# Optimization experiments

Hardware: AMD Instinct MI355X
Metric: run time of the kernel (lower is better)

Reference implementation:

```python
import jax, jax.numpy as jnp
import numpy as np

B, L, D, H, DH = 2, 2048, 1024, 16, 64
THETA_T = 100.0
EPS_COS = 1e-6
EPS_NORM = 1e-6


def make_rope_tables(n_heads=H, d_head=DH, theta_t=THETA_T):
    dr = d_head // 12                      # 5 rotary freqs per head per axis
    n = n_heads * dr
    log_min, log_max = np.log(np.pi), np.log(10.0 * np.pi)
    f = np.exp(np.linspace(log_min, log_max, n + 1)[:-1])
    freqs = np.stack([f, f]).reshape(2, dr, n_heads).transpose(0, 2, 1)   # (2, H, dr)
    t_freqs = (theta_t ** (-np.arange(n, dtype=np.float64) / n)).reshape(dr, n_heads).T  # (H, dr)
    return jnp.asarray(freqs, jnp.float32), jnp.asarray(t_freqs, jnp.float32)


def rms_norm(x, scale, eps=EPS_NORM):
    ms = jnp.mean(x.astype(jnp.float32) ** 2, axis=-1, keepdims=True)
    return x * (scale.astype(jnp.float32) * jax.lax.rsqrt(ms + eps)).astype(x.dtype)


def rope_theta(pos, pos_orig, time, freqs, t_freqs):
    # pos_to_use: (b, l, c=2, xy=2), mapped to [-1, 1]
    pos_use = jnp.stack([pos_orig, pos], axis=2) * 2.0 - 1.0
    theta_w = pos_use[..., 0][:, :, :, None, None] * freqs[0]      # b l 2 H dr
    theta_h = pos_use[..., 1][:, :, :, None, None] * freqs[1]      # b l 2 H dr
    theta_t = time[:, :, None, None, None] * t_freqs               # b l 1 H dr
    theta = jnp.concatenate([theta_h, theta_w, theta_t], axis=2)   # b l 5 H dr
    b, l = theta.shape[0], theta.shape[1]
    theta = jnp.transpose(theta, (0, 1, 3, 2, 4)).reshape(b, l, H, -1)  # b l H (5*dr)
    return theta


def apply_rotary_emb(x, theta):
    d = theta.shape[-1]
    x1, x2, x3 = x[..., :d], x[..., d:2 * d], x[..., 2 * d:]
    cos, sin = jnp.cos(theta), jnp.sin(theta)
    y1 = x1 * cos - x2 * sin
    y2 = x2 * cos + x1 * sin
    return jnp.concatenate([y1, y2, x3], axis=-1)


def scale_for_cosine_sim(q, k, scale, eps=EPS_COS):
    sq = jnp.sum(q * q, axis=-1, keepdims=True)
    sk = jnp.sum(k * k, axis=-1, keepdims=True)
    sqrt_scale = jnp.sqrt(scale)                         # (H,1,1) -> broadcasts to (b,H,l,1)
    return q * (sqrt_scale * jax.lax.rsqrt(sq + eps)), k * (sqrt_scale * jax.lax.rsqrt(sk + eps))


def setup_inputs() -> dict:
    key = jax.random.key(0)
    ks = jax.random.split(key, 8)
    return {
        "x": jax.random.normal(ks[0], (B, L, D), jnp.float32),
        "pos": jax.random.uniform(ks[1], (B, L, 2), jnp.float32),
        "pos_orig": jax.random.uniform(ks[2], (B, L, 2), jnp.float32),
        "time": jax.random.uniform(ks[3], (B, L), jnp.float32),
        "w_qkv": jax.random.normal(ks[4], (3 * D, D), jnp.float32) * (D ** -0.5),
        "w_out": jax.random.normal(ks[5], (D, D), jnp.float32) * (D ** -0.5),
        "w_up": jax.random.normal(ks[6], (4 * D, D), jnp.float32) * (D ** -0.5),
        "w_down": jax.random.normal(ks[7], (D, 4 * D), jnp.float32) * ((4 * D) ** -0.5),
        "norm1_scale": jnp.ones((D,), jnp.float32),
        "norm2_scale": jnp.ones((D,), jnp.float32),
        "qk_scale": jnp.full((H, 1, 1), 10.0, jnp.float32),
    }


def reference(x, pos, pos_orig, time, w_qkv, w_out, w_up, w_down,
              norm1_scale, norm2_scale, qk_scale):
    freqs, t_freqs = make_rope_tables()
    b, l, _ = x.shape

    # --- attention block (pre-norm) ---
    xn = rms_norm(x, norm1_scale)
    qkv = jnp.einsum('bld,ed->ble', xn, w_qkv)                  # b l 3D
    q, k, v = jnp.split(qkv, 3, axis=-1)
    q = q.reshape(b, l, H, DH)
    k = k.reshape(b, l, H, DH)
    v = v.reshape(b, l, H, DH).transpose(0, 2, 1, 3)            # b H l dh

    theta = rope_theta(pos, pos_orig, time, freqs, t_freqs)      # b l H 25
    q = apply_rotary_emb(q, theta).transpose(0, 2, 1, 3)         # b H l dh
    k = apply_rotary_emb(k, theta).transpose(0, 2, 1, 3)

    q, k = scale_for_cosine_sim(q, k, qk_scale)                  # cosine-sim QK norm
    scores = jnp.einsum('bhqd,bhkd->bhqk', q, k)                 # scale=1 (already folded in)
    probs = jax.nn.softmax(scores, axis=-1)
    attn = jnp.einsum('bhqk,bhkd->bhqd', probs, v)
    attn = attn.transpose(0, 2, 1, 3).reshape(b, l, D)
    x = x + jnp.einsum('bld,ed->ble', attn, w_out)

    h = rms_norm(x, norm2_scale)
    h = jax.nn.gelu(jnp.einsum('bld,ed->ble', h, w_up), approximate=True)
    x = x + jnp.einsum('ble,de->bld', h, w_down)
    return x
```

## Files before the change

### kernel.cpp

```cpp
#include <hip/hip_runtime.h>

#define B_ 2
#define L_ 2048
#define D_ 1024
#define H_ 16
#define DH_ 64

typedef float f32x4 __attribute__((ext_vector_type(4)));
typedef __bf16 bf16x8 __attribute__((ext_vector_type(8)));

__device__ __forceinline__ ushort f2bf(float f) {
  unsigned u = __float_as_uint(f);
  u += 0x7fffu + ((u >> 16) & 1u);
  return (ushort)(u >> 16);
}
__device__ __forceinline__ float bf2f(ushort h) {
  return __uint_as_float(((unsigned)h) << 16);
}

__device__ __forceinline__ void gload_lds16(const void* g, void* l) {
  __builtin_amdgcn_global_load_lds(
      (const __attribute__((address_space(1))) unsigned*)g,
      (__attribute__((address_space(3))) unsigned*)l, 16, 0, 0);
}

__global__ __launch_bounds__(256) void cast_bf16_kernel(const float* __restrict__ in,
                                                        ushort* __restrict__ out, int n4) {
  int i = blockIdx.x * 256 + threadIdx.x;
  if (i >= n4) return;
  float4 v = ((const float4*)in)[i];
  ushort4 o;
  o.x = f2bf(v.x); o.y = f2bf(v.y); o.z = f2bf(v.z); o.w = f2bf(v.w);
  ((ushort4*)out)[i] = o;
}

__global__ __launch_bounds__(256) void rmsnorm_kernel(const float* __restrict__ x,
                                                      const float* __restrict__ scale,
                                                      ushort* __restrict__ out) {
  int row = blockIdx.x, t = threadIdx.x;
  float4 v = ((const float4*)(x + (size_t)row * D_))[t];
  float ss = v.x * v.x + v.y * v.y + v.z * v.z + v.w * v.w;
#pragma unroll
  for (int d = 1; d < 64; d <<= 1) ss += __shfl_xor(ss, d);
  __shared__ float wsum[4];
  if ((t & 63) == 0) wsum[t >> 6] = ss;
  __syncthreads();
  float tot = wsum[0] + wsum[1] + wsum[2] + wsum[3];
  float r = rsqrtf(tot * (1.0f / D_) + 1e-6f);
  float4 sc = ((const float4*)scale)[t];
  ushort4 o;
  o.x = f2bf(v.x * sc.x * r); o.y = f2bf(v.y * sc.y * r);
  o.z = f2bf(v.z * sc.z * r); o.w = f2bf(v.w * sc.w * r);
  ((ushort4*)(out + (size_t)row * D_))[t] = o;
}

template <int EPI, int BM, int BN, int DEPTH, int XR>
__global__ __launch_bounds__(256) void gemm_nt(const ushort* __restrict__ A,
                                               const ushort* __restrict__ Bw,
                                               void* __restrict__ Cout,
                                               const float* __restrict__ resid,
                                               int M, int N, int K) {
  constexpr int WROWS = BM / 2, WCOLS = BN / 2;
  constexpr int MR = WROWS / 16, NR = WCOLS / 16;
  constexpr int ALOADS = BM / 64, BLOADS = BN / 64;
  constexpr int NLOADS = ALOADS + BLOADS;
  constexpr int XC = 8 / XR;
  __shared__ __align__(16) ushort Als[DEPTH][BM * 32];
  __shared__ __align__(16) ushort Bls[DEPTH][BN * 32];
  const int tid = threadIdx.x;
  const int lane = tid & 63;
  const int w = tid >> 6;
  const int wr = w >> 1, wc = w & 1;
  const int bid = blockIdx.y * gridDim.x + blockIdx.x;
  const int xcd = bid & 7;
  const int i = bid >> 3;
  const int CR = gridDim.x / XR, CC = gridDim.y / XC;
  const int rt = (xcd % XR) * CR + (i % CR);
  const int ct = (xcd / XR) * CC + (i / CR);
  const int row0 = rt * BM;
  const int col0 = ct * BN;
  const ushort* Ab = A + (size_t)row0 * K;
  const ushort* Bb = Bw + (size_t)col0 * K;
  const int sr = tid >> 2;
  const int scA = (((tid & 3) ^ ((tid >> 3) & 3)) * 8);
  const int fr = lane & 15;
  const int fg = lane >> 4;
  f32x4 zero = {0.f, 0.f, 0.f, 0.f};
  f32x4 acc[MR][NR];
#pragma unroll
  for (int m = 0; m < MR; m++)
#pragma unroll
    for (int n = 0; n < NR; n++) acc[m][n] = zero;

  auto stage = [&](int buf, int kt) {
#pragma unroll
    for (int i2 = 0; i2 < ALOADS; i2++)
      gload_lds16(Ab + (size_t)(sr + 64 * i2) * K + kt + scA, &Als[buf][i2 * 2048 + tid * 8]);
#pragma unroll
    for (int i2 = 0; i2 < BLOADS; i2++)
      gload_lds16(Bb + (size_t)(sr + 64 * i2) * K + kt + scA, &Bls[buf][i2 * 2048 + tid * 8]);
  };
  const int nt = K >> 5;
#pragma unroll
  for (int p = 0; p < DEPTH - 1; p++) stage(p, p << 5);
  int cur = 0, sbuf = DEPTH - 1;
  for (int t = 0; t < nt; t++) {
    const int ahead = nt - 1 - t;
    if constexpr (DEPTH == 3) {
      if (ahead >= 1) asm volatile("s_waitcnt vmcnt(%0)" ::"i"(NLOADS) : "memory");
      else            asm volatile("s_waitcnt vmcnt(0)" ::: "memory");
    } else {
      if (ahead >= 3)      asm volatile("s_waitcnt vmcnt(%0)" ::"i"(3 * NLOADS) : "memory");
      else if (ahead == 2) asm volatile("s_waitcnt vmcnt(%0)" ::"i"(2 * NLOADS) : "memory");
      else if (ahead == 1) asm volatile("s_waitcnt vmcnt(%0)" ::"i"(NLOADS) : "memory");
      else                 asm volatile("s_waitcnt vmcnt(0)" ::: "memory");
    }
    __builtin_amdgcn_s_barrier();
    __builtin_amdgcn_sched_barrier(0);
    if (t + DEPTH - 1 < nt) {
      stage(sbuf, (t + DEPTH - 1) << 5);
      sbuf = (sbuf == DEPTH - 1) ? 0 : sbuf + 1;
    }
    bf16x8 af[MR], bfr[NR];
#pragma unroll
    for (int m = 0; m < MR; m++) {
      int rA = wr * WROWS + m * 16 + fr;
      af[m] = *(const bf16x8*)&Als[cur][rA * 32 + ((fg ^ ((rA >> 1) & 3)) << 3)];
    }
#pragma unroll
    for (int n = 0; n < NR; n++) {
      int rB = wc * WCOLS + n * 16 + fr;
      bfr[n] = *(const bf16x8*)&Bls[cur][rB * 32 + ((fg ^ ((rB >> 1) & 3)) << 3)];
    }
    __builtin_amdgcn_s_setprio(1);
#pragma unroll
    for (int m = 0; m < MR; m++)
#pragma unroll
      for (int n = 0; n < NR; n++)
        acc[m][n] = __builtin_amdgcn_mfma_f32_16x16x32_bf16(af[m], bfr[n], acc[m][n], 0, 0, 0);
    __builtin_amdgcn_s_setprio(0);
    cur = (cur == DEPTH - 1) ? 0 : cur + 1;
  }
  const int orow = row0 + wr * WROWS + fg * 4;
  const int ocol = col0 + wc * WCOLS + fr;
#pragma unroll
  for (int m = 0; m < MR; m++) {
#pragma unroll
    for (int j = 0; j < 4; j++) {
      int r = orow + m * 16 + j;
#pragma unroll
      for (int n = 0; n < NR; n++) {
        int cidx = ocol + n * 16;
        size_t idx = (size_t)r * N + cidx;
        float v = acc[m][n][j];
        if (EPI == 0) {
          ((ushort*)Cout)[idx] = f2bf(v);
        } else if (EPI == 1) {
          ((float*)Cout)[idx] = resid[idx] + v;
        } else {
          float g = 0.5f * v * (1.0f + tanhf(0.7978845608f * (v + 0.044715f * v * v * v)));
          ((ushort*)Cout)[idx] = f2bf(g);
        }
      }
    }
  }
}

__global__ __launch_bounds__(256) void rope_kernel(const ushort* __restrict__ qkv,
                                                   const float* __restrict__ pos,
                                                   const float* __restrict__ pos_orig,
                                                   const float* __restrict__ timep,
                                                   const float* __restrict__ qk_scale,
                                                   ushort* __restrict__ qr,
                                                   ushort* __restrict__ kr) {
  int gw = (blockIdx.x * 256 + threadIdx.x) >> 6;
  int lane = threadIdx.x & 63;
  int h = gw & 15;
  int row = gw >> 4;
  int b = row >> 11;
  int l = row & (L_ - 1);
  float qv = bf2f(qkv[(size_t)row * 3072 + h * 64 + lane]);
  float kv = bf2f(qkv[(size_t)row * 3072 + 1024 + h * 64 + lane]);
  float c = 1.0f, s = 0.0f;
  if (lane < 50) {
    int idx = lane < 25 ? lane : lane - 25;
    int sg = idx / 5, d = idx % 5;
    int fi = d * 16 + h;
    float th;
    if (sg == 4) {
      th = timep[row] * __expf(-(float)fi * 0.05756462732485115f);
    } else {
      float fr = 3.14159265358979323846f * __expf((float)fi * 0.028782313662425575f);
      const float* psrc = (sg == 0 || sg == 2) ? pos_orig : pos;
      int comp = (sg < 2) ? 1 : 0;
      th = (2.0f * psrc[(size_t)row * 2 + comp] - 1.0f) * fr;
    }
    s = sinf(th);
    c = cosf(th);
  }
  int partner = lane < 25 ? lane + 25 : lane - 25;
  float qp = __shfl(qv, partner, 64);
  float kp = __shfl(kv, partner, 64);
  float yq, yk;
  if (lane < 25) { yq = qv * c - qp * s; yk = kv * c - kp * s; }
  else if (lane < 50) { yq = qv * c + qp * s; yk = kv * c + kp * s; }
  else { yq = qv; yk = kv; }
  float sq = yq * yq, sk = yk * yk;
#pragma unroll
  for (int d = 1; d < 64; d <<= 1) { sq += __shfl_xor(sq, d); sk += __shfl_xor(sk, d); }
  float scl = sqrtf(qk_scale[h]);
  float qo = yq * scl * rsqrtf(sq + 1e-6f);
  float ko = yk * scl * rsqrtf(sk + 1e-6f);
  size_t o = ((size_t)(b * 16 + h) * L_ + l) * 64 + lane;
  qr[o] = f2bf(qo);
  kr[o] = f2bf(ko);
}

__global__ __launch_bounds__(256) void vtrans_kernel(const ushort* __restrict__ qkv,
                                                     ushort* __restrict__ vT) {
  __shared__ __align__(16) ushort tile[64][72];
  int t = threadIdx.x;
  int lt = blockIdx.x;
  int bh = blockIdx.y;
  int b = bh >> 4, h = bh & 15;
  int r = t >> 3, c0 = (t & 7) * 8;
#pragma unroll
  for (int half = 0; half < 2; half++) {
    const ushort* src =
        qkv + (size_t)(b * L_ + lt * 64 + r + half * 32) * 3072 + 2048 + h * 64 + c0;
    *(uint4*)&tile[r + half * 32][c0] = *(const uint4*)src;
  }
  __syncthreads();
#pragma unroll
  for (int half = 0; half < 2; half++) {
    int dh = r + half * 32;
    unsigned p0 = (unsigned)tile[c0 + 0][dh] | ((unsigned)tile[c0 + 1][dh] << 16);
    unsigned p1 = (unsigned)tile[c0 + 2][dh] | ((unsigned)tile[c0 + 3][dh] << 16);
    unsigned p2 = (unsigned)tile[c0 + 4][dh] | ((unsigned)tile[c0 + 5][dh] << 16);
    unsigned p3 = (unsigned)tile[c0 + 6][dh] | ((unsigned)tile[c0 + 7][dh] << 16);
    uint4 o; o.x = p0; o.y = p1; o.z = p2; o.w = p3;
    *(uint4*)&vT[((size_t)bh * 64 + dh) * L_ + lt * 64 + c0] = o;
  }
}

__global__ __launch_bounds__(256) void attn_kernel(const ushort* __restrict__ qr,
                                                   const ushort* __restrict__ kr,
                                                   const ushort* __restrict__ vT,
                                                   ushort* __restrict__ attnb) {
  __shared__ __align__(16) ushort Kls[2][64 * 64];
  __shared__ __align__(16) ushort Vls[2][64 * 64];
  __shared__ __align__(16) ushort Pls[4][16 * 64];
  const int tid = threadIdx.x, lane = tid & 63, w = tid >> 6;
  const int qt = blockIdx.x, bh = blockIdx.y;
  const int b = bh >> 4;
  const int fr = lane & 15, fg = lane >> 4;
  const ushort* Qb = qr + ((size_t)bh * L_ + qt * 64 + w * 16) * 64;
  bf16x8 qf[2];
#pragma unroll
  for (int c = 0; c < 2; c++)
    qf[c] = *(const bf16x8*)(Qb + fr * 64 + c * 32 + fg * 8);
  f32x4 zero = {0.f, 0.f, 0.f, 0.f};
  f32x4 accO[4];
#pragma unroll
  for (int n = 0; n < 4; n++) accO[n] = zero;
  float lrow[4] = {0.f, 0.f, 0.f, 0.f};
  const int sr = tid >> 3;
  const int scz = (((tid & 7) ^ (sr & 7)) * 8);
  auto stage = [&](int buf, int kt) {
    gload_lds16(kr + ((size_t)bh * L_ + kt + sr) * 64 + scz, &Kls[buf][tid * 8]);
    gload_lds16(kr + ((size_t)bh * L_ + kt + 32 + sr) * 64 + scz, &Kls[buf][2048 + tid * 8]);
    gload_lds16(vT + ((size_t)bh * 64 + sr) * L_ + kt + scz, &Vls[buf][tid * 8]);
    gload_lds16(vT + ((size_t)bh * 64 + 32 + sr) * L_ + kt + scz, &Vls[buf][2048 + tid * 8]);
  };
  stage(0, 0);
  int cur = 0;
  for (int t = 0; t < (L_ >> 6); t++) {
    asm volatile("s_waitcnt vmcnt(0)" ::: "memory");
    __builtin_amdgcn_s_barrier();
    __builtin_amdgcn_sched_barrier(0);
    if (t + 1 < (L_ >> 6)) stage(cur ^ 1, (t + 1) << 6);
    f32x4 sv[4];
#pragma unroll
    for (int n = 0; n < 4; n++) sv[n] = zero;
    __builtin_amdgcn_s_setprio(1);
#pragma unroll
    for (int c = 0; c < 2; c++) {
#pragma unroll
      for (int n = 0; n < 4; n++) {
        bf16x8 kf =
            *(const bf16x8*)&Kls[cur][(n * 16 + fr) * 64 + (((c * 4 + fg) ^ (fr & 7)) << 3)];
        sv[n] = __builtin_amdgcn_mfma_f32_16x16x32_bf16(qf[c], kf, sv[n], 0, 0, 0);
      }
    }
    __builtin_amdgcn_s_setprio(0);
#pragma unroll
    for (int n = 0; n < 4; n++)
#pragma unroll
      for (int j = 0; j < 4; j++) {
        float p = __expf(sv[n][j] - 12.0f);
        sv[n][j] = p;
        lrow[j] += p;
      }
#pragma unroll
    for (int j = 0; j < 4; j++) {
      int row = fg * 4 + j;
      int rbase = row * 64;
      int rx = row & 7;
#pragma unroll
      for (int n = 0; n < 4; n++) {
        int chunk = 2 * n + (fr >> 3);
        Pls[w][rbase + ((chunk ^ rx) << 3) + (fr & 7)] =
            (ushort)(__float_as_uint(sv[n][j]) >> 16);
      }
    }
    __builtin_amdgcn_s_setprio(1);
#pragma unroll
    for (int c = 0; c < 2; c++) {
      bf16x8 pa = *(const bf16x8*)&Pls[w][fr * 64 + (((c * 4 + fg) ^ (fr & 7)) << 3)];
#pragma unroll
      for (int n = 0; n < 4; n++) {
        bf16x8 vb =
            *(const bf16x8*)&Vls[cur][(n * 16 + fr) * 64 + (((c * 4 + fg) ^ (fr & 7)) << 3)];
        accO[n] = __builtin_amdgcn_mfma_f32_16x16x32_bf16(pa, vb, accO[n], 0, 0, 0);
      }
    }
    __builtin_amdgcn_s_setprio(0);
    cur ^= 1;
  }
#pragma unroll
  for (int j = 0; j < 4; j++) {
#pragma unroll
    for (int d = 1; d < 16; d <<= 1) lrow[j] += __shfl_xor(lrow[j], d);
    lrow[j] = 1.0f / lrow[j];
  }
#pragma unroll
  for (int n = 0; n < 4; n++) {
#pragma unroll
    for (int j = 0; j < 4; j++) {
      float o = accO[n][j] * lrow[j];
      int qrow = qt * 64 + w * 16 + fg * 4 + j;
      int dh = fr + n * 16;
      attnb[(size_t)(b * L_ + qrow) * 1024 + (bh & 15) * 64 + dh] = f2bf(o);
    }
  }
}

extern "C" void kernel_launch(void* const* d_in, const int* in_sizes, int n_in,
                              void* d_out, int out_size, void* d_ws, size_t ws_size,
                              hipStream_t stream) {
  const float* x = (const float*)d_in[0];
  const float* pos = (const float*)d_in[1];
  const float* pos_orig = (const float*)d_in[2];
  const float* timep = (const float*)d_in[3];
  const float* w_qkv = (const float*)d_in[4];
  const float* w_out = (const float*)d_in[5];
  const float* w_up = (const float*)d_in[6];
  const float* w_down = (const float*)d_in[7];
  const float* norm1 = (const float*)d_in[8];
  const float* norm2 = (const float*)d_in[9];
  const float* qk_scale = (const float*)d_in[10];
  float* out = (float*)d_out;
  char* ws = (char*)d_ws;
  size_t off = 0;
  auto alloc = [&](size_t bytes) {
    void* p = ws + off;
    off += bytes;
    return p;
  };
  ushort* xn = (ushort*)alloc(8ull << 20);
  ushort* qkvb = (ushort*)alloc(32ull << 20);
  ushort* qrb = (ushort*)alloc(8ull << 20);
  ushort* krb = (ushort*)alloc(8ull << 20);
  ushort* vTb = (ushort*)alloc(8ull << 20);
  ushort* attnb = (ushort*)alloc(8ull << 20);
  float* x1 = (float*)alloc(16ull << 20);
  ushort* wqkvb = (ushort*)alloc(6ull << 20);
  ushort* woutb = (ushort*)alloc(2ull << 20);
  ushort* wupb = (ushort*)alloc(8ull << 20);
  ushort* wdownb = (ushort*)alloc(8ull << 20);

  cast_bf16_kernel<<<3072, 256, 0, stream>>>(w_qkv, wqkvb, 3145728 / 4);
  cast_bf16_kernel<<<1024, 256, 0, stream>>>(w_out, woutb, 1048576 / 4);
  cast_bf16_kernel<<<4096, 256, 0, stream>>>(w_up, wupb, 4194304 / 4);
  cast_bf16_kernel<<<4096, 256, 0, stream>>>(w_down, wdownb, 4194304 / 4);

  rmsnorm_kernel<<<4096, 256, 0, stream>>>(x, norm1, xn);
  gemm_nt<0, 128, 128, 3, 4><<<dim3(32, 24), 256, 0, stream>>>(xn, wqkvb, qkvb, nullptr, 4096, 3072, 1024);
  rope_kernel<<<16384, 256, 0, stream>>>(qkvb, pos, pos_orig, timep, qk_scale, qrb, krb);
  vtrans_kernel<<<dim3(32, 32), 256, 0, stream>>>(qkvb, vTb);
  attn_kernel<<<dim3(32, 32), 256, 0, stream>>>(qrb, krb, vTb, attnb);
  gemm_nt<1, 64, 64, 5, 8><<<dim3(64, 16), 256, 0, stream>>>(attnb, woutb, x1, x, 4096, 1024, 1024);
  rmsnorm_kernel<<<4096, 256, 0, stream>>>(x1, norm2, xn);
  gemm_nt<2, 128, 128, 3, 4><<<dim3(32, 32), 256, 0, stream>>>(xn, wupb, qkvb, nullptr, 4096, 4096, 1024);
  gemm_nt<1, 64, 64, 5, 8><<<dim3(64, 16), 256, 0, stream>>>(qkvb, wdownb, out, x1, 4096, 1024, 4096);
}
```

Baseline: 299.4 us.

## Merge weight casts, store residual in bf16, and remap GEMM/attention block order

Replaces the four weight-cast launches with one combined kernel. Stores the intermediate residual x1 as bf16 instead of fp32, so the out-projection epilogue, the second rmsnorm and the down-projection epilogue move less data. Changes the XCD tile-mapping parameters of the out and down GEMMs, with an option to make the column index vary fastest, and remaps attention blocks so consecutive blocks on an XCD share a head. Rounding the residual stream to bf16 loses precision in the final output.

```diff
diff --git a/kernel.cpp b/kernel.cpp
--- a/kernel.cpp
+++ b/kernel.cpp
@@ -24,21 +24,40 @@
       (__attribute__((address_space(3))) unsigned*)l, 16, 0, 0);
 }
 
-__global__ __launch_bounds__(256) void cast_bf16_kernel(const float* __restrict__ in,
-                                                        ushort* __restrict__ out, int n4) {
+__global__ __launch_bounds__(256) void cast_all_kernel(const float* __restrict__ w0,
+                                                       const float* __restrict__ w1,
+                                                       const float* __restrict__ w2,
+                                                       const float* __restrict__ w3,
+                                                       ushort* __restrict__ o0,
+                                                       ushort* __restrict__ o1,
+                                                       ushort* __restrict__ o2,
+                                                       ushort* __restrict__ o3) {
   int i = blockIdx.x * 256 + threadIdx.x;
-  if (i >= n4) return;
-  float4 v = ((const float4*)in)[i];
+  const float* src;
+  ushort* dst;
+  int j = i;
+  if (j < 786432) { src = w0; dst = o0; }
+  else if (j < 786432 + 262144) { j -= 786432; src = w1; dst = o1; }
+  else if (j < 786432 + 262144 + 1048576) { j -= 786432 + 262144; src = w2; dst = o2; }
+  else { j -= 786432 + 262144 + 1048576; src = w3; dst = o3; }
+  float4 v = ((const float4*)src)[j];
   ushort4 o;
   o.x = f2bf(v.x); o.y = f2bf(v.y); o.z = f2bf(v.z); o.w = f2bf(v.w);
-  ((ushort4*)out)[i] = o;
-}
-
-__global__ __launch_bounds__(256) void rmsnorm_kernel(const float* __restrict__ x,
+  ((ushort4*)dst)[j] = o;
+}
+
+template <typename T>
+__global__ __launch_bounds__(256) void rmsnorm_kernel(const T* __restrict__ x,
                                                       const float* __restrict__ scale,
                                                       ushort* __restrict__ out) {
   int row = blockIdx.x, t = threadIdx.x;
-  float4 v = ((const float4*)(x + (size_t)row * D_))[t];
+  float4 v;
+  if constexpr (sizeof(T) == 4) {
+    v = ((const float4*)((const float*)x + (size_t)row * D_))[t];
+  } else {
+    ushort4 u = ((const ushort4*)((const ushort*)x + (size_t)row * D_))[t];
+    v.x = bf2f(u.x); v.y = bf2f(u.y); v.z = bf2f(u.z); v.w = bf2f(u.w);
+  }
   float ss = v.x * v.x + v.y * v.y + v.z * v.z + v.w * v.w;
 #pragma unroll
   for (int d = 1; d < 64; d <<= 1) ss += __shfl_xor(ss, d);
@@ -54,17 +73,16 @@
   ((ushort4*)(out + (size_t)row * D_))[t] = o;
 }
 
-template <int EPI, int BM, int BN, int DEPTH, int XR>
+template <int EPI, int BM, int BN, int DEPTH, int XR, int XC, bool CTFAST>
 __global__ __launch_bounds__(256) void gemm_nt(const ushort* __restrict__ A,
                                                const ushort* __restrict__ Bw,
                                                void* __restrict__ Cout,
-                                               const float* __restrict__ resid,
+                                               const void* __restrict__ resid,
                                                int M, int N, int K) {
   constexpr int WROWS = BM / 2, WCOLS = BN / 2;
   constexpr int MR = WROWS / 16, NR = WCOLS / 16;
   constexpr int ALOADS = BM / 64, BLOADS = BN / 64;
   constexpr int NLOADS = ALOADS + BLOADS;
-  constexpr int XC = 8 / XR;
   __shared__ __align__(16) ushort Als[DEPTH][BM * 32];
   __shared__ __align__(16) ushort Bls[DEPTH][BN * 32];
   const int tid = threadIdx.x;
@@ -73,10 +91,16 @@
   const int wr = w >> 1, wc = w & 1;
   const int bid = blockIdx.y * gridDim.x + blockIdx.x;
   const int xcd = bid & 7;
-  const int i = bid >> 3;
+  const int i0 = bid >> 3;
   const int CR = gridDim.x / XR, CC = gridDim.y / XC;
-  const int rt = (xcd % XR) * CR + (i % CR);
-  const int ct = (xcd / XR) * CC + (i / CR);
+  int rt, ct;
+  if constexpr (CTFAST) {
+    rt = (xcd % XR) * CR + (i0 / CC);
+    ct = (xcd / XR) * CC + (i0 % CC);
+  } else {
+    rt = (xcd % XR) * CR + (i0 % CR);
+    ct = (xcd / XR) * CC + (i0 / CR);
+  }
   const int row0 = rt * BM;
   const int col0 = ct * BN;
   const ushort* Ab = A + (size_t)row0 * K;
@@ -92,13 +116,13 @@
 #pragma unroll
     for (int n = 0; n < NR; n++) acc[m][n] = zero;
 
-  auto stage = [&](int buf, int kt) {
+  auto stage = [&](int slot, int kt) {
 #pragma unroll
     for (int i2 = 0; i2 < ALOADS; i2++)
-      gload_lds16(Ab + (size_t)(sr + 64 * i2) * K + kt + scA, &Als[buf][i2 * 2048 + tid * 8]);
+      gload_lds16(Ab + (size_t)(sr + 64 * i2) * K + kt + scA, &Als[slot][i2 * 2048 + tid * 8]);
 #pragma unroll
     for (int i2 = 0; i2 < BLOADS; i2++)
-      gload_lds16(Bb + (size_t)(sr + 64 * i2) * K + kt + scA, &Bls[buf][i2 * 2048 + tid * 8]);
+      gload_lds16(Bb + (size_t)(sr + 64 * i2) * K + kt + scA, &Bls[slot][i2 * 2048 + tid * 8]);
   };
   const int nt = K >> 5;
 #pragma unroll
@@ -156,10 +180,12 @@
         if (EPI == 0) {
           ((ushort*)Cout)[idx] = f2bf(v);
         } else if (EPI == 1) {
-          ((float*)Cout)[idx] = resid[idx] + v;
-        } else {
+          ((ushort*)Cout)[idx] = f2bf(((const float*)resid)[idx] + v);
+        } else if (EPI == 2) {
           float g = 0.5f * v * (1.0f + tanhf(0.7978845608f * (v + 0.044715f * v * v * v)));
           ((ushort*)Cout)[idx] = f2bf(g);
+        } else {
+          ((float*)Cout)[idx] = bf2f(((const ushort*)resid)[idx]) + v;
         }
       }
     }
@@ -251,7 +277,9 @@
   __shared__ __align__(16) ushort Vls[2][64 * 64];
   __shared__ __align__(16) ushort Pls[4][16 * 64];
   const int tid = threadIdx.x, lane = tid & 63, w = tid >> 6;
-  const int qt = blockIdx.x, bh = blockIdx.y;
+  const int bid = blockIdx.y * gridDim.x + blockIdx.x;
+  const int qt = (bid >> 3) & 31;
+  const int bh = (bid & 7) | ((bid >> 8) << 3);
   const int b = bh >> 4;
   const int fr = lane & 15, fg = lane >> 4;
   const ushort* Qb = qr + ((size_t)bh * L_ + qt * 64 + w * 16) * 64;
@@ -373,24 +401,26 @@
   ushort* krb = (ushort*)alloc(8ull << 20);
   ushort* vTb = (ushort*)alloc(8ull << 20);
   ushort* attnb = (ushort*)alloc(8ull << 20);
-  float* x1 = (float*)alloc(16ull << 20);
+  ushort* x1b = (ushort*)alloc(8ull << 20);
   ushort* wqkvb = (ushort*)alloc(6ull << 20);
   ushort* woutb = (ushort*)alloc(2ull << 20);
   ushort* wupb = (ushort*)alloc(8ull << 20);
   ushort* wdownb = (ushort*)alloc(8ull << 20);
 
-  cast_bf16_kernel<<<3072, 256, 0, stream>>>(w_qkv, wqkvb, 3145728 / 4);
-  cast_bf16_kernel<<<1024, 256, 0, stream>>>(w_out, woutb, 1048576 / 4);
-  cast_bf16_kernel<<<4096, 256, 0, stream>>>(w_up, wupb, 4194304 / 4);
-  cast_bf16_kernel<<<4096, 256, 0, stream>>>(w_down, wdownb, 4194304 / 4);
-
-  rmsnorm_kernel<<<4096, 256, 0, stream>>>(x, norm1, xn);
-  gemm_nt<0, 128, 128, 3, 4><<<dim3(32, 24), 256, 0, stream>>>(xn, wqkvb, qkvb, nullptr, 4096, 3072, 1024);
+  cast_all_kernel<<<12288, 256, 0, stream>>>(w_qkv, w_out, w_up, w_down,
+                                             wqkvb, woutb, wupb, wdownb);
+
+  rmsnorm_kernel<float><<<4096, 256, 0, stream>>>(x, norm1, xn);
+  gemm_nt<0, 128, 128, 3, 4, 2, false><<<dim3(32, 24), 256, 0, stream>>>(
+      xn, wqkvb, qkvb, nullptr, 4096, 3072, 1024);
   rope_kernel<<<16384, 256, 0, stream>>>(qkvb, pos, pos_orig, timep, qk_scale, qrb, krb);
   vtrans_kernel<<<dim3(32, 32), 256, 0, stream>>>(qkvb, vTb);
   attn_kernel<<<dim3(32, 32), 256, 0, stream>>>(qrb, krb, vTb, attnb);
-  gemm_nt<1, 64, 64, 5, 8><<<dim3(64, 16), 256, 0, stream>>>(attnb, woutb, x1, x, 4096, 1024, 1024);
-  rmsnorm_kernel<<<4096, 256, 0, stream>>>(x1, norm2, xn);
-  gemm_nt<2, 128, 128, 3, 4><<<dim3(32, 32), 256, 0, stream>>>(xn, wupb, qkvb, nullptr, 4096, 4096, 1024);
-  gemm_nt<1, 64, 64, 5, 8><<<dim3(64, 16), 256, 0, stream>>>(qkvb, wdownb, out, x1, 4096, 1024, 4096);
-}
+  gemm_nt<1, 64, 64, 5, 4, 2, false><<<dim3(64, 16), 256, 0, stream>>>(
+      attnb, woutb, x1b, x, 4096, 1024, 1024);
+  rmsnorm_kernel<ushort><<<4096, 256, 0, stream>>>(x1b, norm2, xn);
+  gemm_nt<2, 128, 128, 3, 4, 2, false><<<dim3(32, 32), 256, 0, stream>>>(
+      xn, wupb, qkvb, nullptr, 4096, 4096, 1024);
+  gemm_nt<3, 64, 64, 5, 4, 2, true><<<dim3(64, 16), 256, 0, stream>>>(
+      qkvb, wdownb, out, x1b, 4096, 1024, 4096);
+}
```

After: 293.2 us. 1.02x faster.
